# Kernel optimization log

Hardware: AMD Instinct MI355X
Metric: run time of the kernel (lower is better)

The kernel has to match this reference:

```python
import jax, jax.numpy as jnp
import numpy as np

H = 50  # hidden size

def setup_inputs() -> dict:
    key = jax.random.key(0)
    k_in, k_wx, k_wh, k_wd = jax.random.split(key, 4)
    B, T, D = 1024, 2048, 1
    inputs = jax.random.normal(k_in, (B, T, D), dtype=jnp.float32)
    # fused gate weights, gate order (i, f, g, o) -> 4H columns
    Wx = jax.random.normal(k_wx, (D, 4 * H), dtype=jnp.float32) * 0.1
    Wh = jax.random.normal(k_wh, (H, 4 * H), dtype=jnp.float32) * 0.1
    b = jnp.zeros((4 * H,), dtype=jnp.float32)
    Wd = jax.random.normal(k_wd, (H, 1), dtype=jnp.float32) * 0.1
    bd = jnp.zeros((1,), dtype=jnp.float32)
    return {"inputs": inputs, "Wx": Wx, "Wh": Wh, "b": b, "Wd": Wd, "bd": bd}

def _lstm_last_hidden(inputs, Wx, Wh, b):
    B = inputs.shape[0]
    c0 = jnp.zeros((B, H), dtype=inputs.dtype)
    h0 = jnp.zeros((B, H), dtype=inputs.dtype)

    def step(carry, x_t):
        c, h = carry
        z = x_t @ Wx + h @ Wh + b          # [B, 4H]
        i, f, g, o = jnp.split(z, 4, axis=-1)
        i = jax.nn.sigmoid(i)
        f = jax.nn.sigmoid(f)
        g = jnp.tanh(g)
        o = jax.nn.sigmoid(o)
        c_new = f * c + i * g
        h_new = o * jnp.tanh(c_new)
        return (c_new, h_new), None

    xs = jnp.swapaxes(inputs, 0, 1)        # [T, B, D] for scan over time
    (c_fin, h_fin), _ = jax.lax.scan(step, (c0, h0), xs)
    return h_fin                            # [B, H]

def reference(inputs, Wx, Wh, b, Wd, bd):
    h_last = _lstm_last_hidden(inputs, Wx, Wh, b)
    return h_last @ Wd + bd                # [B, 1]
```

## Files before the change

### kernel.cpp

```cpp
#include <hip/hip_runtime.h>
#include <hip/hip_bf16.h>

#define HID 50
#define FOURH 200
#define TSTEPS 2048
#define NBATCH 1024

typedef _Float16 v2h __attribute__((ext_vector_type(2)));

#define LOG2E 1.44269504f

__device__ __forceinline__ float frcp(float x)  { return __builtin_amdgcn_rcpf(x); }
__device__ __forceinline__ float fexp2(float x) { return __builtin_amdgcn_exp2f(x); }

__device__ __forceinline__ float fast_sigmoid(float x) {
    return frcp(1.0f + fexp2(-LOG2E * x));
}
__device__ __forceinline__ float fast_tanh(float x) {
    return 1.0f - 2.0f * frcp(fexp2((2.0f * LOG2E) * x) + 1.0f);
}

__device__ __forceinline__ v2h bc_v2h(unsigned int u) {
    return __builtin_bit_cast(v2h, u);
}

__global__ __launch_bounds__(64, 1)
void lstm_dot2_kernel(const float* __restrict__ x,
                      const float* __restrict__ Wx,
                      const float* __restrict__ Wh,
                      const float* __restrict__ bias,
                      const float* __restrict__ Wd,
                      const float* __restrict__ bd,
                      float* __restrict__ out) {
    const int b    = blockIdx.x;
    const int lane = threadIdx.x;
    const int lc   = (lane < HID) ? lane : (HID - 1);

    __shared__ __align__(16) float    xs[TSTEPS + 4];
    __shared__ __align__(16) _Float16 hbuf[80];

    const float4* xb4 = (const float4*)(x + (size_t)b * TSTEPS);
    float4* xs4 = (float4*)xs;
    #pragma unroll
    for (int i = lane; i < TSTEPS / 4; i += 64) xs4[i] = xb4[i];
    if (lane == 0) xs[TSTEPS] = 0.0f;
    for (int i = lane; i < 80; i += 64) hbuf[i] = (_Float16)0.0f;

    v2h wi[25], wf[25], wg[25], wo[25];
    #pragma unroll
    for (int k2 = 0; k2 < 25; ++k2) {
        const float* r0 = Wh + (2 * k2) * FOURH;
        const float* r1 = Wh + (2 * k2 + 1) * FOURH;
        wi[k2] = v2h{(_Float16)r0[lc],           (_Float16)r1[lc]};
        wf[k2] = v2h{(_Float16)r0[HID + lc],     (_Float16)r1[HID + lc]};
        wg[k2] = v2h{(_Float16)r0[2 * HID + lc], (_Float16)r1[2 * HID + lc]};
        wo[k2] = v2h{(_Float16)r0[3 * HID + lc], (_Float16)r1[3 * HID + lc]};
    }
    const float wx_i = Wx[lc],           b_i = bias[lc];
    const float wx_f = Wx[HID + lc],     b_f = bias[HID + lc];
    const float wx_g = Wx[2 * HID + lc], b_g = bias[2 * HID + lc];
    const float wx_o = Wx[3 * HID + lc], b_o = bias[3 * HID + lc];

    const int widx = (lane < HID) ? lane : (lane + 14);

    float c = 0.0f;
    float h = 0.0f;
    __syncthreads();

    const uint4* hb4 = (const uint4*)hbuf;
    float xt = xs[0];

    for (int t = 0; t < TSTEPS; ++t) {
        const float xt_next = xs[t + 1];
        const uint4 q0 = hb4[0], q1 = hb4[1], q2 = hb4[2], q3 = hb4[3];
        const uint4 q4 = hb4[4], q5 = hb4[5], q6 = hb4[6];
        unsigned int hr[28] = {q0.x, q0.y, q0.z, q0.w, q1.x, q1.y, q1.z, q1.w,
                               q2.x, q2.y, q2.z, q2.w, q3.x, q3.y, q3.z, q3.w,
                               q4.x, q4.y, q4.z, q4.w, q5.x, q5.y, q5.z, q5.w,
                               q6.x, q6.y, q6.z, q6.w};
        float ai0 = 0.f, ai1 = 0.f, af0 = 0.f, af1 = 0.f;
        float ag0 = 0.f, ag1 = 0.f, ao0 = 0.f, ao1 = 0.f;
        #pragma unroll
        for (int j = 0; j < 12; ++j) {
            const v2h hp0 = bc_v2h(hr[2 * j]);
            const v2h hp1 = bc_v2h(hr[2 * j + 1]);
            ai0 = __builtin_amdgcn_fdot2(wi[2 * j],     hp0, ai0, false);
            af0 = __builtin_amdgcn_fdot2(wf[2 * j],     hp0, af0, false);
            ag0 = __builtin_amdgcn_fdot2(wg[2 * j],     hp0, ag0, false);
            ao0 = __builtin_amdgcn_fdot2(wo[2 * j],     hp0, ao0, false);
            ai1 = __builtin_amdgcn_fdot2(wi[2 * j + 1], hp1, ai1, false);
            af1 = __builtin_amdgcn_fdot2(wf[2 * j + 1], hp1, af1, false);
            ag1 = __builtin_amdgcn_fdot2(wg[2 * j + 1], hp1, ag1, false);
            ao1 = __builtin_amdgcn_fdot2(wo[2 * j + 1], hp1, ao1, false);
        }
        {
            const v2h hp = bc_v2h(hr[24]);
            ai0 = __builtin_amdgcn_fdot2(wi[24], hp, ai0, false);
            af0 = __builtin_amdgcn_fdot2(wf[24], hp, af0, false);
            ag0 = __builtin_amdgcn_fdot2(wg[24], hp, ag0, false);
            ao0 = __builtin_amdgcn_fdot2(wo[24], hp, ao0, false);
        }
        const float zi = fmaf(xt, wx_i, b_i) + (ai0 + ai1);
        const float zf = fmaf(xt, wx_f, b_f) + (af0 + af1);
        const float zg = fmaf(xt, wx_g, b_g) + (ag0 + ag1);
        const float zo = fmaf(xt, wx_o, b_o) + (ao0 + ao1);

        const float ig = fast_sigmoid(zi);
        const float fg = fast_sigmoid(zf);
        const float gg = fast_tanh(zg);
        const float og = fast_sigmoid(zo);
        c = fmaf(fg, c, ig * gg);
        h = og * fast_tanh(c);

        hbuf[widx] = (_Float16)h;
        xt = xt_next;
    }

    float v = (lane < HID) ? h * Wd[lane] : 0.0f;
    #pragma unroll
    for (int off = 32; off > 0; off >>= 1) v += __shfl_down(v, off);
    if (lane == 0) out[b] = v + bd[0];
}

extern "C" void kernel_launch(void* const* d_in, const int* in_sizes, int n_in,
                              void* d_out, int out_size, void* d_ws, size_t ws_size,
                              hipStream_t stream) {
    const float* x    = (const float*)d_in[0];
    const float* Wx   = (const float*)d_in[1];
    const float* Wh   = (const float*)d_in[2];
    const float* bias = (const float*)d_in[3];
    const float* Wd   = (const float*)d_in[4];
    const float* bd   = (const float*)d_in[5];
    float* out = (float*)d_out;

    lstm_dot2_kernel<<<dim3(NBATCH), dim3(64), 0, stream>>>(
        x, Wx, Wh, bias, Wd, bd, out);
}
```

Before: 786.9 us.

## Broadcast hidden state via DPP and readlane instead of LDS round-trip

Each step now builds packed fp16 hidden pairs in registers: a DPP row shift pulls the neighbouring lane's value, and 25 readlane ops broadcast the pairs as scalars for the fdot2 loop. This removes the per-step LDS store and vector loads of the hidden state, along with their wait latency. LOG2E is also folded into the weights and bias so the gate activations skip one multiply each. The risks are that 25 serialized readlanes per step may cost more than the LDS traffic, and that fp16 rounding of the prescaled weights changes results slightly.

New measurement: 751.7 us. 1.05x faster.

```diff
diff --git a/kernel.cpp b/kernel.cpp
--- a/kernel.cpp
+++ b/kernel.cpp
@@ -1,5 +1,4 @@
 #include <hip/hip_runtime.h>
-#include <hip/hip_bf16.h>
 
 #define HID 50
 #define FOURH 200
@@ -13,8 +12,11 @@
 __device__ __forceinline__ float frcp(float x)  { return __builtin_amdgcn_rcpf(x); }
 __device__ __forceinline__ float fexp2(float x) { return __builtin_amdgcn_exp2f(x); }
 
-__device__ __forceinline__ float fast_sigmoid(float x) {
-    return frcp(1.0f + fexp2(-LOG2E * x));
+__device__ __forceinline__ float sigmoid_p(float zp) {
+    return frcp(1.0f + fexp2(-zp));
+}
+__device__ __forceinline__ float tanh_p(float zp) {
+    return 1.0f - 2.0f * frcp(fexp2(2.0f * zp) + 1.0f);
 }
 __device__ __forceinline__ float fast_tanh(float x) {
     return 1.0f - 2.0f * frcp(fexp2((2.0f * LOG2E) * x) + 1.0f);
@@ -25,94 +27,94 @@
 }
 
 __global__ __launch_bounds__(64, 1)
-void lstm_dot2_kernel(const float* __restrict__ x,
-                      const float* __restrict__ Wx,
-                      const float* __restrict__ Wh,
-                      const float* __restrict__ bias,
-                      const float* __restrict__ Wd,
-                      const float* __restrict__ bd,
-                      float* __restrict__ out) {
+void lstm_rlane_kernel(const float* __restrict__ x,
+                       const float* __restrict__ Wx,
+                       const float* __restrict__ Wh,
+                       const float* __restrict__ bias,
+                       const float* __restrict__ Wd,
+                       const float* __restrict__ bd,
+                       float* __restrict__ out) {
     const int b    = blockIdx.x;
     const int lane = threadIdx.x;
     const int lc   = (lane < HID) ? lane : (HID - 1);
 
-    __shared__ __align__(16) float    xs[TSTEPS + 4];
-    __shared__ __align__(16) _Float16 hbuf[80];
+    __shared__ __align__(16) float xs[TSTEPS + 4];
 
     const float4* xb4 = (const float4*)(x + (size_t)b * TSTEPS);
     float4* xs4 = (float4*)xs;
     #pragma unroll
     for (int i = lane; i < TSTEPS / 4; i += 64) xs4[i] = xb4[i];
     if (lane == 0) xs[TSTEPS] = 0.0f;
-    for (int i = lane; i < 80; i += 64) hbuf[i] = (_Float16)0.0f;
 
     v2h wi[25], wf[25], wg[25], wo[25];
     #pragma unroll
     for (int k2 = 0; k2 < 25; ++k2) {
         const float* r0 = Wh + (2 * k2) * FOURH;
         const float* r1 = Wh + (2 * k2 + 1) * FOURH;
-        wi[k2] = v2h{(_Float16)r0[lc],           (_Float16)r1[lc]};
-        wf[k2] = v2h{(_Float16)r0[HID + lc],     (_Float16)r1[HID + lc]};
-        wg[k2] = v2h{(_Float16)r0[2 * HID + lc], (_Float16)r1[2 * HID + lc]};
-        wo[k2] = v2h{(_Float16)r0[3 * HID + lc], (_Float16)r1[3 * HID + lc]};
+        wi[k2] = v2h{(_Float16)(LOG2E * r0[lc]),           (_Float16)(LOG2E * r1[lc])};
+        wf[k2] = v2h{(_Float16)(LOG2E * r0[HID + lc]),     (_Float16)(LOG2E * r1[HID + lc])};
+        wg[k2] = v2h{(_Float16)(LOG2E * r0[2 * HID + lc]), (_Float16)(LOG2E * r1[2 * HID + lc])};
+        wo[k2] = v2h{(_Float16)(LOG2E * r0[3 * HID + lc]), (_Float16)(LOG2E * r1[3 * HID + lc])};
     }
-    const float wx_i = Wx[lc],           b_i = bias[lc];
-    const float wx_f = Wx[HID + lc],     b_f = bias[HID + lc];
-    const float wx_g = Wx[2 * HID + lc], b_g = bias[2 * HID + lc];
-    const float wx_o = Wx[3 * HID + lc], b_o = bias[3 * HID + lc];
-
-    const int widx = (lane < HID) ? lane : (lane + 14);
+    const float wx_i = LOG2E * Wx[lc],           b_i = LOG2E * bias[lc];
+    const float wx_f = LOG2E * Wx[HID + lc],     b_f = LOG2E * bias[HID + lc];
+    const float wx_g = LOG2E * Wx[2 * HID + lc], b_g = LOG2E * bias[2 * HID + lc];
+    const float wx_o = LOG2E * Wx[3 * HID + lc], b_o = LOG2E * bias[3 * HID + lc];
 
     float c = 0.0f;
     float h = 0.0f;
     __syncthreads();
 
-    const uint4* hb4 = (const uint4*)hbuf;
     float xt = xs[0];
 
     for (int t = 0; t < TSTEPS; ++t) {
         const float xt_next = xs[t + 1];
-        const uint4 q0 = hb4[0], q1 = hb4[1], q2 = hb4[2], q3 = hb4[3];
-        const uint4 q4 = hb4[4], q5 = hb4[5], q6 = hb4[6];
-        unsigned int hr[28] = {q0.x, q0.y, q0.z, q0.w, q1.x, q1.y, q1.z, q1.w,
-                               q2.x, q2.y, q2.z, q2.w, q3.x, q3.y, q3.z, q3.w,
-                               q4.x, q4.y, q4.z, q4.w, q5.x, q5.y, q5.z, q5.w,
-                               q6.x, q6.y, q6.z, q6.w};
+
+        const unsigned h16  = (unsigned)__builtin_bit_cast(unsigned short, (_Float16)h);
+        const unsigned h16n = (unsigned)__builtin_amdgcn_update_dpp(
+            0, (int)h16, 0x101 , 0xf, 0xf, true);
+        const unsigned hp = h16 | (h16n << 16);
+
+        unsigned sh[25];
+        #pragma unroll
+        for (int k = 0; k < 25; ++k)
+            sh[k] = (unsigned)__builtin_amdgcn_readlane((int)hp, 2 * k);
+
         float ai0 = 0.f, ai1 = 0.f, af0 = 0.f, af1 = 0.f;
         float ag0 = 0.f, ag1 = 0.f, ao0 = 0.f, ao1 = 0.f;
         #pragma unroll
         for (int j = 0; j < 12; ++j) {
-            const v2h hp0 = bc_v2h(hr[2 * j]);
-            const v2h hp1 = bc_v2h(hr[2 * j + 1]);
-            ai0 = __builtin_amdgcn_fdot2(wi[2 * j],     hp0, ai0, false);
-            af0 = __builtin_amdgcn_fdot2(wf[2 * j],     hp0, af0, false);
-            ag0 = __builtin_amdgcn_fdot2(wg[2 * j],     hp0, ag0, false);
-            ao0 = __builtin_amdgcn_fdot2(wo[2 * j],     hp0, ao0, false);
-            ai1 = __builtin_amdgcn_fdot2(wi[2 * j + 1], hp1, ai1, false);
-            af1 = __builtin_amdgcn_fdot2(wf[2 * j + 1], hp1, af1, false);
-            ag1 = __builtin_amdgcn_fdot2(wg[2 * j + 1], hp1, ag1, false);
-            ao1 = __builtin_amdgcn_fdot2(wo[2 * j + 1], hp1, ao1, false);
+            const v2h h0 = bc_v2h(sh[2 * j]);
+            const v2h h1 = bc_v2h(sh[2 * j + 1]);
+            ai0 = __builtin_amdgcn_fdot2(wi[2 * j],     h0, ai0, false);
+            af0 = __builtin_amdgcn_fdot2(wf[2 * j],     h0, af0, false);
+            ag0 = __builtin_amdgcn_fdot2(wg[2 * j],     h0, ag0, false);
+            ao0 = __builtin_amdgcn_fdot2(wo[2 * j],     h0, ao0, false);
+            ai1 = __builtin_amdgcn_fdot2(wi[2 * j + 1], h1, ai1, false);
+            af1 = __builtin_amdgcn_fdot2(wf[2 * j + 1], h1, af1, false);
+            ag1 = __builtin_amdgcn_fdot2(wg[2 * j + 1], h1, ag1, false);
+            ao1 = __builtin_amdgcn_fdot2(wo[2 * j + 1], h1, ao1, false);
         }
         {
-            const v2h hp = bc_v2h(hr[24]);
-            ai0 = __builtin_amdgcn_fdot2(wi[24], hp, ai0, false);
-            af0 = __builtin_amdgcn_fdot2(wf[24], hp, af0, false);
-            ag0 = __builtin_amdgcn_fdot2(wg[24], hp, ag0, false);
-            ao0 = __builtin_amdgcn_fdot2(wo[24], hp, ao0, false);
+            const v2h hp24 = bc_v2h(sh[24]);
+            ai0 = __builtin_amdgcn_fdot2(wi[24], hp24, ai0, false);
+            af0 = __builtin_amdgcn_fdot2(wf[24], hp24, af0, false);
+            ag0 = __builtin_amdgcn_fdot2(wg[24], hp24, ag0, false);
+            ao0 = __builtin_amdgcn_fdot2(wo[24], hp24, ao0, false);
         }
+
         const float zi = fmaf(xt, wx_i, b_i) + (ai0 + ai1);
         const float zf = fmaf(xt, wx_f, b_f) + (af0 + af1);
         const float zg = fmaf(xt, wx_g, b_g) + (ag0 + ag1);
         const float zo = fmaf(xt, wx_o, b_o) + (ao0 + ao1);
 
-        const float ig = fast_sigmoid(zi);
-        const float fg = fast_sigmoid(zf);
-        const float gg = fast_tanh(zg);
-        const float og = fast_sigmoid(zo);
+        const float ig = sigmoid_p(zi);
+        const float fg = sigmoid_p(zf);
+        const float gg = tanh_p(zg);
+        const float og = sigmoid_p(zo);
         c = fmaf(fg, c, ig * gg);
         h = og * fast_tanh(c);
 
-        hbuf[widx] = (_Float16)h;
         xt = xt_next;
     }
 
@@ -133,6 +135,6 @@
     const float* bd   = (const float*)d_in[5];
     float* out = (float*)d_out;
 
-    lstm_dot2_kernel<<<dim3(NBATCH), dim3(64), 0, stream>>>(
+    lstm_rlane_kernel<<<dim3(NBATCH), dim3(64), 0, stream>>>(
         x, Wx, Wh, bias, Wd, bd, out);
 }
```

## Compute recurrent gate matvec with MFMA 16x16x32 f16 instead of dot2

Applied to the files above, without the earlier changes.

Replaces the per-lane fdot2 recurrent matvec (100 dot2 per step) with 32 MFMA 16x16x32 f16 instructions, where h is broadcast as the A operand and the weight columns are permuted into B fragments held in registers. Each lane picks its gate values out of the accumulator rows with selects. It also folds the log2e scaling into the weights, Wx and bias, which removes a multiply before each exp2. The MFMA approach computes a 16-row matrix product for a single useful row and adds MFMA latency to the serial time chain.

Result: slower. 884.8 us (+12.5%).

```diff
diff --git a/kernel.cpp b/kernel.cpp
--- a/kernel.cpp
+++ b/kernel.cpp
@@ -1,31 +1,20 @@
 #include <hip/hip_runtime.h>
-#include <hip/hip_bf16.h>
 
 #define HID 50
 #define FOURH 200
 #define TSTEPS 2048
 #define NBATCH 1024
 
-typedef _Float16 v2h __attribute__((ext_vector_type(2)));
+#define LOG2E 1.44269504f
 
-#define LOG2E 1.44269504f
+typedef _Float16 half8 __attribute__((ext_vector_type(8)));
+typedef float    f32x4 __attribute__((ext_vector_type(4)));
 
 __device__ __forceinline__ float frcp(float x)  { return __builtin_amdgcn_rcpf(x); }
 __device__ __forceinline__ float fexp2(float x) { return __builtin_amdgcn_exp2f(x); }
 
-__device__ __forceinline__ float fast_sigmoid(float x) {
-    return frcp(1.0f + fexp2(-LOG2E * x));
-}
-__device__ __forceinline__ float fast_tanh(float x) {
-    return 1.0f - 2.0f * frcp(fexp2((2.0f * LOG2E) * x) + 1.0f);
-}
-
-__device__ __forceinline__ v2h bc_v2h(unsigned int u) {
-    return __builtin_bit_cast(v2h, u);
-}
-
 __global__ __launch_bounds__(64, 1)
-void lstm_dot2_kernel(const float* __restrict__ x,
+void lstm_mfma_kernel(const float* __restrict__ x,
                       const float* __restrict__ Wx,
                       const float* __restrict__ Wh,
                       const float* __restrict__ bias,
@@ -34,6 +23,8 @@
                       float* __restrict__ out) {
     const int b    = blockIdx.x;
     const int lane = threadIdx.x;
+    const int g    = lane >> 4;
+    const int cl   = lane & 15;
     const int lc   = (lane < HID) ? lane : (HID - 1);
 
     __shared__ __align__(16) float    xs[TSTEPS + 4];
@@ -46,20 +37,31 @@
     if (lane == 0) xs[TSTEPS] = 0.0f;
     for (int i = lane; i < 80; i += 64) hbuf[i] = (_Float16)0.0f;
 
-    v2h wi[25], wf[25], wg[25], wo[25];
+    half8 bf[32];
     #pragma unroll
-    for (int k2 = 0; k2 < 25; ++k2) {
-        const float* r0 = Wh + (2 * k2) * FOURH;
-        const float* r1 = Wh + (2 * k2 + 1) * FOURH;
-        wi[k2] = v2h{(_Float16)r0[lc],           (_Float16)r1[lc]};
-        wf[k2] = v2h{(_Float16)r0[HID + lc],     (_Float16)r1[HID + lc]};
-        wg[k2] = v2h{(_Float16)r0[2 * HID + lc], (_Float16)r1[2 * HID + lc]};
-        wo[k2] = v2h{(_Float16)r0[3 * HID + lc], (_Float16)r1[3 * HID + lc]};
+    for (int n = 0; n < 16; ++n) {
+        const int cp = 16 * n + cl;
+        const int w  = cp >> 6;
+        const int u  = cp & 63;
+        const float sc = (w == 2) ? (2.0f * LOG2E) : LOG2E;
+        #pragma unroll
+        for (int s = 0; s < 2; ++s) {
+            half8 hb;
+            #pragma unroll
+            for (int j = 0; j < 8; ++j) {
+                const int k = s * 32 + g * 8 + j;
+                float v = 0.0f;
+                if (k < HID && u < HID) v = sc * Wh[k * FOURH + w * HID + u];
+                hb[j] = (_Float16)v;
+            }
+            bf[2 * n + s] = hb;
+        }
     }
-    const float wx_i = Wx[lc],           b_i = bias[lc];
-    const float wx_f = Wx[HID + lc],     b_f = bias[HID + lc];
-    const float wx_g = Wx[2 * HID + lc], b_g = bias[2 * HID + lc];
-    const float wx_o = Wx[3 * HID + lc], b_o = bias[3 * HID + lc];
+
+    const float wx_i = LOG2E * Wx[lc],                  b_i = LOG2E * bias[lc];
+    const float wx_f = LOG2E * Wx[HID + lc],            b_f = LOG2E * bias[HID + lc];
+    const float wx_g = 2.0f * LOG2E * Wx[2 * HID + lc], b_g = 2.0f * LOG2E * bias[2 * HID + lc];
+    const float wx_o = LOG2E * Wx[3 * HID + lc],        b_o = LOG2E * bias[3 * HID + lc];
 
     const int widx = (lane < HID) ? lane : (lane + 14);
 
@@ -67,50 +69,59 @@
     float h = 0.0f;
     __syncthreads();
 
-    const uint4* hb4 = (const uint4*)hbuf;
     float xt = xs[0];
+    const f32x4 zero4 = {0.0f, 0.0f, 0.0f, 0.0f};
 
     for (int t = 0; t < TSTEPS; ++t) {
         const float xt_next = xs[t + 1];
-        const uint4 q0 = hb4[0], q1 = hb4[1], q2 = hb4[2], q3 = hb4[3];
-        const uint4 q4 = hb4[4], q5 = hb4[5], q6 = hb4[6];
-        unsigned int hr[28] = {q0.x, q0.y, q0.z, q0.w, q1.x, q1.y, q1.z, q1.w,
-                               q2.x, q2.y, q2.z, q2.w, q3.x, q3.y, q3.z, q3.w,
-                               q4.x, q4.y, q4.z, q4.w, q5.x, q5.y, q5.z, q5.w,
-                               q6.x, q6.y, q6.z, q6.w};
-        float ai0 = 0.f, ai1 = 0.f, af0 = 0.f, af1 = 0.f;
-        float ag0 = 0.f, ag1 = 0.f, ao0 = 0.f, ao1 = 0.f;
+
+        const half8 a0 = *(const half8*)(hbuf + g * 8);
+        const half8 a1 = *(const half8*)(hbuf + 32 + g * 8);
+
+        f32x4 acc[16];
         #pragma unroll
-        for (int j = 0; j < 12; ++j) {
-            const v2h hp0 = bc_v2h(hr[2 * j]);
-            const v2h hp1 = bc_v2h(hr[2 * j + 1]);
-            ai0 = __builtin_amdgcn_fdot2(wi[2 * j],     hp0, ai0, false);
-            af0 = __builtin_amdgcn_fdot2(wf[2 * j],     hp0, af0, false);
-            ag0 = __builtin_amdgcn_fdot2(wg[2 * j],     hp0, ag0, false);
-            ao0 = __builtin_amdgcn_fdot2(wo[2 * j],     hp0, ao0, false);
-            ai1 = __builtin_amdgcn_fdot2(wi[2 * j + 1], hp1, ai1, false);
-            af1 = __builtin_amdgcn_fdot2(wf[2 * j + 1], hp1, af1, false);
-            ag1 = __builtin_amdgcn_fdot2(wg[2 * j + 1], hp1, ag1, false);
-            ao1 = __builtin_amdgcn_fdot2(wo[2 * j + 1], hp1, ao1, false);
+        for (int n = 0; n < 16; ++n)
+            acc[n] = __builtin_amdgcn_mfma_f32_16x16x32_f16(a0, bf[2 * n], zero4, 0, 0, 0);
+        #pragma unroll
+        for (int n = 0; n < 16; ++n)
+            acc[n] = __builtin_amdgcn_mfma_f32_16x16x32_f16(a1, bf[2 * n + 1], acc[n], 0, 0, 0);
+
+        const bool g1 = (g & 1) != 0;
+        const bool g2 = (g & 2) != 0;
+        float zd0, zd1, zd2, zd3;
+        {
+            const float v01 = g1 ? acc[1][0]  : acc[0][0];
+            const float v23 = g1 ? acc[3][0]  : acc[2][0];
+            zd0 = g2 ? v23 : v01;
         }
         {
-            const v2h hp = bc_v2h(hr[24]);
-            ai0 = __builtin_amdgcn_fdot2(wi[24], hp, ai0, false);
-            af0 = __builtin_amdgcn_fdot2(wf[24], hp, af0, false);
-            ag0 = __builtin_amdgcn_fdot2(wg[24], hp, ag0, false);
-            ao0 = __builtin_amdgcn_fdot2(wo[24], hp, ao0, false);
+            const float v01 = g1 ? acc[5][0]  : acc[4][0];
+            const float v23 = g1 ? acc[7][0]  : acc[6][0];
+            zd1 = g2 ? v23 : v01;
         }
-        const float zi = fmaf(xt, wx_i, b_i) + (ai0 + ai1);
-        const float zf = fmaf(xt, wx_f, b_f) + (af0 + af1);
-        const float zg = fmaf(xt, wx_g, b_g) + (ag0 + ag1);
-        const float zo = fmaf(xt, wx_o, b_o) + (ao0 + ao1);
+        {
+            const float v01 = g1 ? acc[9][0]  : acc[8][0];
+            const float v23 = g1 ? acc[11][0] : acc[10][0];
+            zd2 = g2 ? v23 : v01;
+        }
+        {
+            const float v01 = g1 ? acc[13][0] : acc[12][0];
+            const float v23 = g1 ? acc[15][0] : acc[14][0];
+            zd3 = g2 ? v23 : v01;
+        }
 
-        const float ig = fast_sigmoid(zi);
-        const float fg = fast_sigmoid(zf);
-        const float gg = fast_tanh(zg);
-        const float og = fast_sigmoid(zo);
+        const float zi = fmaf(xt, wx_i, b_i) + zd0;
+        const float zf = fmaf(xt, wx_f, b_f) + zd1;
+        const float zg = fmaf(xt, wx_g, b_g) + zd2;
+        const float zo = fmaf(xt, wx_o, b_o) + zd3;
+
+        const float ig = frcp(1.0f + fexp2(-zi));
+        const float fg = frcp(1.0f + fexp2(-zf));
+        const float og = frcp(1.0f + fexp2(-zo));
+        const float gg = fmaf(-2.0f, frcp(fexp2(zg) + 1.0f), 1.0f);
         c = fmaf(fg, c, ig * gg);
-        h = og * fast_tanh(c);
+        const float tc = fmaf(-2.0f, frcp(fexp2((2.0f * LOG2E) * c) + 1.0f), 1.0f);
+        h = og * tc;
 
         hbuf[widx] = (_Float16)h;
         xt = xt_next;
@@ -133,6 +144,6 @@
     const float* bd   = (const float*)d_in[5];
     float* out = (float*)d_out;
 
-    lstm_dot2_kernel<<<dim3(NBATCH), dim3(64), 0, stream>>>(
+    lstm_mfma_kernel<<<dim3(NBATCH), dim3(64), 0, stream>>>(
         x, Wx, Wh, bias, Wd, bd, out);
 }
```

## Split LSTM gate computation across two waves with LDS exchange

Applied to the files above, without the earlier changes.

Each batch row now runs as two wavefronts: one computes the i and f gates, the other g and o, which halves each wave's dot-product work per timestep. The activation scale factors are folded into the fp16 recurrent weights, input weights and bias, so sigmoid and tanh share one exp2+rcp form. Partial activations are swapped through shared memory and both waves redundantly update c and h. This costs two block barriers per timestep on a 2048-step serial chain. Doubling the wave count may also improve latency hiding on the CU.

Measured after the change: 1.049 ms. 1.33x slower.

```diff
diff --git a/kernel.cpp b/kernel.cpp
--- a/kernel.cpp
+++ b/kernel.cpp
@@ -1,65 +1,62 @@
 #include <hip/hip_runtime.h>
-#include <hip/hip_bf16.h>
 
 #define HID 50
 #define FOURH 200
 #define TSTEPS 2048
 #define NBATCH 1024
 
+#define LOG2E 1.44269504f
+
 typedef _Float16 v2h __attribute__((ext_vector_type(2)));
-
-#define LOG2E 1.44269504f
 
 __device__ __forceinline__ float frcp(float x)  { return __builtin_amdgcn_rcpf(x); }
 __device__ __forceinline__ float fexp2(float x) { return __builtin_amdgcn_exp2f(x); }
-
-__device__ __forceinline__ float fast_sigmoid(float x) {
-    return frcp(1.0f + fexp2(-LOG2E * x));
-}
-__device__ __forceinline__ float fast_tanh(float x) {
-    return 1.0f - 2.0f * frcp(fexp2((2.0f * LOG2E) * x) + 1.0f);
-}
-
 __device__ __forceinline__ v2h bc_v2h(unsigned int u) {
     return __builtin_bit_cast(v2h, u);
 }
 
-__global__ __launch_bounds__(64, 1)
-void lstm_dot2_kernel(const float* __restrict__ x,
-                      const float* __restrict__ Wx,
-                      const float* __restrict__ Wh,
-                      const float* __restrict__ bias,
-                      const float* __restrict__ Wd,
-                      const float* __restrict__ bd,
-                      float* __restrict__ out) {
+__global__ __launch_bounds__(128, 1)
+void lstm_2wave_kernel(const float* __restrict__ x,
+                       const float* __restrict__ Wx,
+                       const float* __restrict__ Wh,
+                       const float* __restrict__ bias,
+                       const float* __restrict__ Wd,
+                       const float* __restrict__ bd,
+                       float* __restrict__ out) {
     const int b    = blockIdx.x;
-    const int lane = threadIdx.x;
+    const int tid  = threadIdx.x;
+    const int wv   = tid >> 6;
+    const int lane = tid & 63;
     const int lc   = (lane < HID) ? lane : (HID - 1);
 
     __shared__ __align__(16) float    xs[TSTEPS + 4];
     __shared__ __align__(16) _Float16 hbuf[80];
+    __shared__ __align__(16) float    exch[256];
 
     const float4* xb4 = (const float4*)(x + (size_t)b * TSTEPS);
     float4* xs4 = (float4*)xs;
     #pragma unroll
-    for (int i = lane; i < TSTEPS / 4; i += 64) xs4[i] = xb4[i];
-    if (lane == 0) xs[TSTEPS] = 0.0f;
-    for (int i = lane; i < 80; i += 64) hbuf[i] = (_Float16)0.0f;
+    for (int i = tid; i < TSTEPS / 4; i += 128) xs4[i] = xb4[i];
+    if (tid == 0) xs[TSTEPS] = 0.0f;
+    for (int i = tid; i < 80; i += 128) hbuf[i] = (_Float16)0.0f;
 
-    v2h wi[25], wf[25], wg[25], wo[25];
+    const int   colA = (wv == 0) ? lc : (2 * HID + lc);
+    const int   colB = (wv == 0) ? (HID + lc) : (3 * HID + lc);
+    const float scA  = (wv == 0) ? -LOG2E : (2.0f * LOG2E);
+    const float scB  = -LOG2E;
+    const float mA   = (wv == 0) ? 1.0f : -2.0f;
+    const float aA   = (wv == 0) ? 0.0f : 1.0f;
+
+    v2h wA[25], wB[25];
     #pragma unroll
-    for (int k2 = 0; k2 < 25; ++k2) {
-        const float* r0 = Wh + (2 * k2) * FOURH;
-        const float* r1 = Wh + (2 * k2 + 1) * FOURH;
-        wi[k2] = v2h{(_Float16)r0[lc],           (_Float16)r1[lc]};
-        wf[k2] = v2h{(_Float16)r0[HID + lc],     (_Float16)r1[HID + lc]};
-        wg[k2] = v2h{(_Float16)r0[2 * HID + lc], (_Float16)r1[2 * HID + lc]};
-        wo[k2] = v2h{(_Float16)r0[3 * HID + lc], (_Float16)r1[3 * HID + lc]};
+    for (int p = 0; p < 25; ++p) {
+        const float* r0 = Wh + (2 * p) * FOURH;
+        const float* r1 = Wh + (2 * p + 1) * FOURH;
+        wA[p] = v2h{(_Float16)(scA * r0[colA]), (_Float16)(scA * r1[colA])};
+        wB[p] = v2h{(_Float16)(scB * r0[colB]), (_Float16)(scB * r1[colB])};
     }
-    const float wx_i = Wx[lc],           b_i = bias[lc];
-    const float wx_f = Wx[HID + lc],     b_f = bias[HID + lc];
-    const float wx_g = Wx[2 * HID + lc], b_g = bias[2 * HID + lc];
-    const float wx_o = Wx[3 * HID + lc], b_o = bias[3 * HID + lc];
+    const float wxA = scA * Wx[colA], bsA = scA * bias[colA];
+    const float wxB = scB * Wx[colB], bsB = scB * bias[colB];
 
     const int widx = (lane < HID) ? lane : (lane + 14);
 
@@ -68,58 +65,69 @@
     __syncthreads();
 
     const uint4* hb4 = (const uint4*)hbuf;
+    float* exch_w = exch + wv * 128;
+    const float* exch_r = exch + (wv ^ 1) * 128;
+
     float xt = xs[0];
 
     for (int t = 0; t < TSTEPS; ++t) {
         const float xt_next = xs[t + 1];
+
         const uint4 q0 = hb4[0], q1 = hb4[1], q2 = hb4[2], q3 = hb4[3];
         const uint4 q4 = hb4[4], q5 = hb4[5], q6 = hb4[6];
         unsigned int hr[28] = {q0.x, q0.y, q0.z, q0.w, q1.x, q1.y, q1.z, q1.w,
                                q2.x, q2.y, q2.z, q2.w, q3.x, q3.y, q3.z, q3.w,
                                q4.x, q4.y, q4.z, q4.w, q5.x, q5.y, q5.z, q5.w,
                                q6.x, q6.y, q6.z, q6.w};
-        float ai0 = 0.f, ai1 = 0.f, af0 = 0.f, af1 = 0.f;
-        float ag0 = 0.f, ag1 = 0.f, ao0 = 0.f, ao1 = 0.f;
+
+        float aA0 = 0.f, aA1 = 0.f, aB0 = 0.f, aB1 = 0.f;
         #pragma unroll
         for (int j = 0; j < 12; ++j) {
-            const v2h hp0 = bc_v2h(hr[2 * j]);
-            const v2h hp1 = bc_v2h(hr[2 * j + 1]);
-            ai0 = __builtin_amdgcn_fdot2(wi[2 * j],     hp0, ai0, false);
-            af0 = __builtin_amdgcn_fdot2(wf[2 * j],     hp0, af0, false);
-            ag0 = __builtin_amdgcn_fdot2(wg[2 * j],     hp0, ag0, false);
-            ao0 = __builtin_amdgcn_fdot2(wo[2 * j],     hp0, ao0, false);
-            ai1 = __builtin_amdgcn_fdot2(wi[2 * j + 1], hp1, ai1, false);
-            af1 = __builtin_amdgcn_fdot2(wf[2 * j + 1], hp1, af1, false);
-            ag1 = __builtin_amdgcn_fdot2(wg[2 * j + 1], hp1, ag1, false);
-            ao1 = __builtin_amdgcn_fdot2(wo[2 * j + 1], hp1, ao1, false);
+            const v2h h0 = bc_v2h(hr[2 * j]);
+            const v2h h1 = bc_v2h(hr[2 * j + 1]);
+            aA0 = __builtin_amdgcn_fdot2(wA[2 * j],     h0, aA0, false);
+            aB0 = __builtin_amdgcn_fdot2(wB[2 * j],     h0, aB0, false);
+            aA1 = __builtin_amdgcn_fdot2(wA[2 * j + 1], h1, aA1, false);
+            aB1 = __builtin_amdgcn_fdot2(wB[2 * j + 1], h1, aB1, false);
         }
         {
             const v2h hp = bc_v2h(hr[24]);
-            ai0 = __builtin_amdgcn_fdot2(wi[24], hp, ai0, false);
-            af0 = __builtin_amdgcn_fdot2(wf[24], hp, af0, false);
-            ag0 = __builtin_amdgcn_fdot2(wg[24], hp, ag0, false);
-            ao0 = __builtin_amdgcn_fdot2(wo[24], hp, ao0, false);
+            aA0 = __builtin_amdgcn_fdot2(wA[24], hp, aA0, false);
+            aB0 = __builtin_amdgcn_fdot2(wB[24], hp, aB0, false);
         }
-        const float zi = fmaf(xt, wx_i, b_i) + (ai0 + ai1);
-        const float zf = fmaf(xt, wx_f, b_f) + (af0 + af1);
-        const float zg = fmaf(xt, wx_g, b_g) + (ag0 + ag1);
-        const float zo = fmaf(xt, wx_o, b_o) + (ao0 + ao1);
 
-        const float ig = fast_sigmoid(zi);
-        const float fg = fast_sigmoid(zf);
-        const float gg = fast_tanh(zg);
-        const float og = fast_sigmoid(zo);
-        c = fmaf(fg, c, ig * gg);
-        h = og * fast_tanh(c);
+        const float zA = fmaf(xt, wxA, bsA) + (aA0 + aA1);
+        const float zB = fmaf(xt, wxB, bsB) + (aB0 + aB1);
 
-        hbuf[widx] = (_Float16)h;
+        const float sA   = frcp(1.0f + fexp2(zA));
+        const float actA = fmaf(mA, sA, aA);
+        const float actB = frcp(1.0f + fexp2(zB));
+
+        exch_w[lane]      = actA;
+        exch_w[64 + lane] = actB;
+        __syncthreads();
+        const float pA = exch_r[lane];
+        const float pB = exch_r[64 + lane];
+
+        const float prod = actA * pA;
+        const float fg   = (wv == 0) ? actB : pB;
+        const float og   = (wv == 0) ? pB   : actB;
+
+        c = fmaf(fg, c, prod);
+        const float tc = fmaf(-2.0f, frcp(1.0f + fexp2((2.0f * LOG2E) * c)), 1.0f);
+        h = og * tc;
+
+        if (wv == 0) hbuf[widx] = (_Float16)h;
+        __syncthreads();
         xt = xt_next;
     }
 
-    float v = (lane < HID) ? h * Wd[lane] : 0.0f;
-    #pragma unroll
-    for (int off = 32; off > 0; off >>= 1) v += __shfl_down(v, off);
-    if (lane == 0) out[b] = v + bd[0];
+    if (wv == 0) {
+        float v = (lane < HID) ? h * Wd[lane] : 0.0f;
+        #pragma unroll
+        for (int off = 32; off > 0; off >>= 1) v += __shfl_down(v, off);
+        if (lane == 0) out[b] = v + bd[0];
+    }
 }
 
 extern "C" void kernel_launch(void* const* d_in, const int* in_sizes, int n_in,
@@ -133,6 +141,6 @@
     const float* bd   = (const float*)d_in[5];
     float* out = (float*)d_out;
 
-    lstm_dot2_kernel<<<dim3(NBATCH), dim3(64), 0, stream>>>(
+    lstm_2wave_kernel<<<dim3(NBATCH), dim3(128), 0, stream>>>(
         x, Wx, Wh, bias, Wd, bd, out);
 }
```
